# Performance work log

Hardware: AMD Instinct MI355X
Metric: run time of the kernel (lower is better)

Reference implementation:

```python
import jax, jax.numpy as jnp
import numpy as np

H = 512
W = 512
N_STROKES = 5000
S = 10          # samples_per_curve
K = 20          # strokes_per_pixel
CANVAS_COLOR = 0.5  # 'gray'
COARSE = 5      # coarse grid downsample factor (H//5, W//5)


def setup_inputs() -> dict:
    key = jax.random.key(0)
    ks = jax.random.split(key, 6)
    # stroke centers spread over the canvas
    location = jax.random.uniform(ks[0], (N_STROKES, 2), jnp.float32) * jnp.array([H, W], jnp.float32)
    # bezier control-point offsets relative to the stroke center
    curve_s = jax.random.normal(ks[1], (N_STROKES, 2), jnp.float32) * 8.0
    curve_e = jax.random.normal(ks[2], (N_STROKES, 2), jnp.float32) * 8.0
    curve_c = jax.random.normal(ks[3], (N_STROKES, 2), jnp.float32) * 8.0
    color = jax.random.uniform(ks[4], (N_STROKES, 3), jnp.float32)
    width = jax.random.uniform(ks[5], (N_STROKES, 1), jnp.float32) * 4.0 + 1.0
    return {"curve_s": curve_s, "curve_e": curve_e, "curve_c": curve_c,
            "color": color, "location": location, "width": width}


def _bezier_points(s, c, e, num_points):
    # s, c, e: [N, 2] -> [N, num_points, 2]
    t = jnp.linspace(0.0, 1.0, num_points).astype(jnp.float32)  # [S]
    omt2 = (1.0 - t) ** 2  # [S]
    t2 = t ** 2
    # x/y computed identically: c + (1-t)^2 (s - c) + t^2 (e - c)
    pts = c[:, None, :] + omt2[None, :, None] * (s - c)[:, None, :] \
          + t2[None, :, None] * (e - c)[:, None, :]
    return pts  # [N, S, 2]


def _nearest_upsample_idx(out_size, in_size):
    # torch F.interpolate mode='nearest': src = floor(dst * in/out)
    idx = jnp.floor(jnp.arange(out_size) * (in_size / out_size)).astype(jnp.int32)
    return jnp.clip(idx, 0, in_size - 1)


def reference(curve_s, curve_e, curve_c, color, location, width):
    # sample bezier curve points (absolute coords)
    pts = _bezier_points(curve_s + location, curve_c + location,
                         curve_e + location, S)  # [N, S, 2]

    # ---- coarse-grid KNN over stroke centers ----
    Hc, Wc = H // COARSE, W // COARSE
    tH = jnp.linspace(0.0, float(H), Hc).astype(jnp.float32)
    tW = jnp.linspace(0.0, float(W), Wc).astype(jnp.float32)
    Px, Py = jnp.meshgrid(tH, tW, indexing='ij')
    P = jnp.stack([Px, Py], axis=-1)  # [Hc, Wc, 2]
    D_centers = jnp.sum(jnp.square(P[:, :, None, :] - location), axis=-1)  # [Hc, Wc, N]
    _, idcs = jax.lax.top_k(-D_centers, K)  # [Hc, Wc, K]

    near_pts = pts[idcs]      # [Hc, Wc, K, S, 2]
    near_col = color[idcs]    # [Hc, Wc, K, 3]
    near_w = width[idcs]      # [Hc, Wc, K, 1]

    # ---- upsample coarse gathers to full res ----
    ih = _nearest_upsample_idx(H, Hc)
    iw = _nearest_upsample_idx(W, Wc)
    near_pts = near_pts[ih][:, iw]   # [H, W, K, S, 2] (nearest)
    near_col = near_col[ih][:, iw]   # [H, W, K, 3]   (nearest)
    # widths: bilinear (align_corners=False, no antialias) per channel
    near_w = jax.image.resize(near_w[..., 0], (H, W, K), method='linear')[..., None]  # [H, W, K, 1]

    # ---- full-res pixel grid ----
    tHf = jnp.linspace(0.0, float(H), H).astype(jnp.float32)
    tWf = jnp.linspace(0.0, float(W), W).astype(jnp.float32)
    Pxf, Pyf = jnp.meshgrid(tHf, tWf, indexing='ij')
    P_full = jnp.stack([Pxf, Pyf], axis=-1)  # [H, W, 2]

    # ---- per-pixel closest point on each polyline segment ----
    a = near_pts[:, :, :, :S - 1, :]              # [H, W, K, S-1, 2]
    b_a = near_pts[:, :, :, 1:, :] - a            # segment direction
    pa = P_full[:, :, None, None, :] - a          # pixel - segment start
    t = jnp.sum(b_a * pa, axis=-1) / jnp.sum(jnp.square(b_a), axis=-1)
    t = jnp.clip(t, 0.0, 1.0)
    closest = a + t[..., None] * b_a
    dist = jnp.sum(jnp.square(P_full[:, :, None, None, :] - closest), axis=-1)  # [H, W, K, S-1]

    D = jnp.min(dist, axis=(-1, -2))  # [H, W]
    min_per_stroke = jnp.min(dist, axis=-1)  # [H, W, K]
    ranking = jax.nn.softmax(100000.0 * (1.0 / (1e-08 + min_per_stroke)), axis=-1)  # [H, W, K]

    I_colors = jnp.einsum('hwkf,hwk->hwf', near_col, ranking)  # [H, W, 3]
    bs = jnp.einsum('hwkf,hwk->hwf', near_w, ranking)          # [H, W, 1]
    bs_mask = jax.nn.sigmoid(bs - D[..., None])
    canvas = jnp.full_like(I_colors, CANVAS_COLOR)
    I = I_colors * bs_mask + (1.0 - bs_mask) * canvas
    return I
```

## Files before the change

### kernel.cpp

```cpp
#include <hip/hip_runtime.h>
#include <math.h>

#define NS 5000
#define SS 10
#define KK 20
#define HC 102
#define NBIN 32
#define BINW 16.0f
#define CAP 192

#define WAVE_SYNC() __asm__ volatile("s_waitcnt lgkmcnt(0)" ::: "memory")

__global__ void prep_kernel(const float* __restrict__ cs, const float* __restrict__ ce,
                            const float* __restrict__ cc, const float* __restrict__ loc,
                            const float* __restrict__ color, const float* __restrict__ width,
                            float* __restrict__ sdata, float4* __restrict__ ctab,
                            int* __restrict__ binCnt) {
    int i = blockIdx.x * 256 + threadIdx.x;
    if (i >= NS) return;
    float lx = loc[i*2+0], ly = loc[i*2+1];
    float sx = cs[i*2+0] + lx, sy = cs[i*2+1] + ly;
    float ex = ce[i*2+0] + lx, ey = ce[i*2+1] + ly;
    float px = cc[i*2+0] + lx, py = cc[i*2+1] + ly;
    float qx[SS], qy[SS];
    #pragma unroll
    for (int j = 0; j < SS; ++j) {
        float tt = (float)j * (1.0f / 9.0f);
        float omt = 1.0f - tt;
        float omt2 = omt * omt, t2 = tt * tt;
        qx[j] = px + omt2 * (sx - px) + t2 * (ex - px);
        qy[j] = py + omt2 * (sy - py) + t2 * (ey - py);
        sdata[i*32 + 2*j + 0] = qx[j];
        sdata[i*32 + 2*j + 1] = qy[j];
    }
    #pragma unroll
    for (int sg = 0; sg < 9; ++sg) {
        float bx = qx[sg+1] - qx[sg], by = qy[sg+1] - qy[sg];
        sdata[i*32 + 20 + sg] = 1.0f / (bx*bx + by*by);
    }
    sdata[i*32 + 29] = 0.0f; sdata[i*32 + 30] = 0.0f; sdata[i*32 + 31] = 0.0f;
    ctab[i] = make_float4(color[i*3+0], color[i*3+1], color[i*3+2], width[i]);
    int b0 = min(max((int)(lx * (1.0f/BINW)), 0), NBIN-1);
    int b1 = min(max((int)(ly * (1.0f/BINW)), 0), NBIN-1);
    atomicAdd(&binCnt[b0*NBIN + b1], 1);
}

__global__ void binscan_kernel(const int* __restrict__ binCnt, int* __restrict__ binStart) {
    __shared__ int wsum[4];
    int t = threadIdx.x;
    int lane = t & 63, w = t >> 6;
    int4 v = ((const int4*)binCnt)[t];
    int s0 = v.x, s1 = s0 + v.y, s2 = s1 + v.z, s3 = s2 + v.w;
    int x = s3;
    #pragma unroll
    for (int off = 1; off < 64; off <<= 1) {
        int y = __shfl_up(x, off, 64);
        if (lane >= off) x += y;
    }
    if (lane == 63) wsum[w] = x;
    __syncthreads();
    int woff = 0;
    #pragma unroll
    for (int i = 0; i < 4; ++i) woff += (i < w) ? wsum[i] : 0;
    int texcl = woff + x - s3;
    binStart[4*t+1] = texcl + s0;
    binStart[4*t+2] = texcl + s1;
    binStart[4*t+3] = texcl + s2;
    binStart[4*t+4] = texcl + s3;
    if (t == 0) binStart[0] = 0;
}

__global__ void binscatter_kernel(const float* __restrict__ loc, const int* __restrict__ binStart,
                                  int* __restrict__ binFill, float2* __restrict__ sxy,
                                  int* __restrict__ sid) {
    int i = blockIdx.x * 256 + threadIdx.x;
    if (i >= NS) return;
    float l0 = loc[i*2+0], l1 = loc[i*2+1];
    int b0 = min(max((int)(l0 * (1.0f/BINW)), 0), NBIN-1);
    int b1 = min(max((int)(l1 * (1.0f/BINW)), 0), NBIN-1);
    int b = b0*NBIN + b1;
    int pos = binStart[b] + atomicAdd(&binFill[b], 1);
    sxy[pos] = make_float2(l0, l1);
    sid[pos] = i;
}

__global__ void __launch_bounds__(256) topk_kernel(const float* __restrict__ loc,
                                                   const float* __restrict__ width,
                                                   const float2* __restrict__ sxy,
                                                   const int* __restrict__ sid,
                                                   const int* __restrict__ binStart,
                                                   int* __restrict__ idcs,
                                                   float* __restrict__ wk) {
    __shared__ unsigned long long sk[4][CAP];
    int w = threadIdx.x >> 6, lane = threadIdx.x & 63;
    int cell = blockIdx.x * 4 + w;
    int ci = cell / HC, cj = cell - ci * HC;
    const float dc = 512.0f / 101.0f;
    float c0 = (float)ci * dc;
    float c1 = (float)cj * dc;
    unsigned long long below = (1ull << lane) - 1ull;

    float R = 30.0f;
    int cnt = 0;
    for (int attempt = 0; attempt < 5; ++attempt) {
        float R2 = R * R;
        int base = 0;
        int by0 = max((int)((c0 - R) * (1.0f/BINW)), 0);
        int by1 = min((int)((c0 + R) * (1.0f/BINW)), NBIN-1);
        int bx0 = max((int)((c1 - R) * (1.0f/BINW)), 0);
        int bx1 = min((int)((c1 + R) * (1.0f/BINW)), NBIN-1);
        for (int by = by0; by <= by1; ++by) {
            int s = binStart[by*NBIN + bx0];
            int e = binStart[by*NBIN + bx1 + 1];
            for (int t0 = s; t0 < e; t0 += 64) {
                int t = t0 + lane;
                int tc = min(t, e - 1);
                float2 p = sxy[tc];
                float dx = c0 - p.x, dy = c1 - p.y;
                float d = dx*dx + dy*dy;
                bool pred = (t < e) && (d < R2);
                unsigned long long mask = __ballot(pred);
                int pos = base + __popcll(mask & below);
                if (pred && pos < CAP)
                    sk[w][pos] = ((unsigned long long)__float_as_uint(d) << 32)
                               | (unsigned int)sid[tc];
                base += __popcll(mask);
            }
        }
        cnt = base;
        if (cnt >= KK) break;
        R *= 1.6f;
    }
    WAVE_SYNC();

    if (cnt >= KK && cnt <= CAP) {
        if (cnt <= 64) {
            unsigned long long k0 = (lane < cnt) ? sk[w][lane] : ~0ull;
            int r0 = 0;
            int j = 0;
            #pragma unroll 1
            for (; j + 4 <= cnt; j += 4) {
                unsigned long long a = sk[w][j],   b = sk[w][j+1];
                unsigned long long c = sk[w][j+2], d = sk[w][j+3];
                r0 += (int)(a < k0) + (int)(b < k0) + (int)(c < k0) + (int)(d < k0);
            }
            for (; j < cnt; ++j) r0 += (int)(sk[w][j] < k0);
            if (r0 < KK && lane < cnt) {
                int idx = (int)(unsigned int)(k0 & 0xffffffffull);
                idcs[cell*KK + r0] = idx;
                wk[cell*KK + r0]   = width[idx];
            }
        } else {
            unsigned long long k0 = (lane       < cnt) ? sk[w][lane]       : ~0ull;
            unsigned long long k1 = (lane + 64  < cnt) ? sk[w][lane + 64]  : ~0ull;
            unsigned long long k2 = (lane + 128 < cnt) ? sk[w][lane + 128] : ~0ull;
            int r0 = 0, r1 = 0, r2 = 0;
            #pragma unroll 1
            for (int j = 0; j < cnt; ++j) {
                unsigned long long a = sk[w][j];
                r0 += (int)(a < k0); r1 += (int)(a < k1); r2 += (int)(a < k2);
            }
            if (r0 < KK && lane < cnt) {
                int idx = (int)(unsigned int)(k0 & 0xffffffffull);
                idcs[cell*KK + r0] = idx;  wk[cell*KK + r0] = width[idx];
            }
            if (r1 < KK && lane + 64 < cnt) {
                int idx = (int)(unsigned int)(k1 & 0xffffffffull);
                idcs[cell*KK + r1] = idx;  wk[cell*KK + r1] = width[idx];
            }
            if (r2 < KK && lane + 128 < cnt) {
                int idx = (int)(unsigned int)(k2 & 0xffffffffull);
                idcs[cell*KK + r2] = idx;  wk[cell*KK + r2] = width[idx];
            }
        }
    } else {
        if (lane == 0) {
            float bd[KK]; int bi[KK];
            for (int k = 0; k < KK; ++k) { bd[k] = 3.4e38f; bi[k] = 0; }
            for (int n = 0; n < NS; ++n) {
                float dx = c0 - loc[n*2+0];
                float dy = c1 - loc[n*2+1];
                float d = dx*dx + dy*dy;
                if (d < bd[KK-1]) {
                    int p = KK - 1;
                    while (p > 0 && bd[p-1] > d) { bd[p] = bd[p-1]; bi[p] = bi[p-1]; --p; }
                    bd[p] = d; bi[p] = n;
                }
            }
            for (int k = 0; k < KK; ++k) {
                idcs[cell*KK + k] = bi[k];
                wk[cell*KK + k]   = width[bi[k]];
            }
        }
    }
}

__global__ void __launch_bounds__(256, 4) render_kernel(const float* __restrict__ sdata,
                                                        const float4* __restrict__ ctab,
                                                        const int* __restrict__ idcs,
                                                        const float* __restrict__ wk,
                                                        float* __restrict__ out) {
    int tt0 = threadIdx.x, lane = tt0 & 63, wq = tt0 >> 6;
    int x = blockIdx.x * 16 + ((wq & 1) << 3) + (lane & 7);
    int y = blockIdx.y * 16 + ((wq >> 1) << 3) + (lane >> 3);
    const float df = 512.0f / 511.0f;
    float p0 = (float)y * df;
    float p1 = (float)x * df;
    int cy = (y * 51) >> 8;
    int cx = (x * 51) >> 8;

    const int4* mip = (const int4*)(idcs + (cy * HC + cx) * KK);
    int4 m0 = mip[0], m1 = mip[1], m2 = mip[2], m3 = mip[3], m4 = mip[4];
    int idxs[KK] = {m0.x,m0.y,m0.z,m0.w, m1.x,m1.y,m1.z,m1.w, m2.x,m2.y,m2.z,m2.w,
                    m3.x,m3.y,m3.z,m3.w, m4.x,m4.y,m4.z,m4.w};

    const float sc = 102.0f / 512.0f;
    float iny = ((float)y + 0.5f) * sc - 0.5f;
    float inx = ((float)x + 0.5f) * sc - 0.5f;
    float y0f = floorf(iny), x0f = floorf(inx);
    float fy = iny - y0f, fx = inx - x0f;
    int y0 = min(max((int)y0f, 0), HC - 1);
    int y1 = min(max((int)y0f + 1, 0), HC - 1);
    int x0 = min(max((int)x0f, 0), HC - 1);
    int x1 = min(max((int)x0f + 1, 0), HC - 1);
    const float* w00 = wk + (y0 * HC + x0) * KK;
    const float* w01 = wk + (y0 * HC + x1) * KK;
    const float* w10 = wk + (y1 * HC + x0) * KK;
    const float* w11 = wk + (y1 * HC + x1) * KK;

    float m = -INFINITY, s = 0.0f;
    float a0 = 0.0f, a1 = 0.0f, a2 = 0.0f, wa = 0.0f;
    float D = INFINITY;

    #pragma unroll 4
    for (int k = 0; k < KK; ++k) {
        const float4* sp = (const float4*)(sdata + idxs[k] * 32);
        float4 f0 = sp[0], f1 = sp[1], f2 = sp[2], f3 = sp[3], f4 = sp[4];
        float4 i0 = sp[5], i1 = sp[6], i2 = sp[7];
        float4 cw = ctab[idxs[k]];
        float qx[10] = {f0.x, f0.z, f1.x, f1.z, f2.x, f2.z, f3.x, f3.z, f4.x, f4.z};
        float qy[10] = {f0.y, f0.w, f1.y, f1.w, f2.y, f2.w, f3.y, f3.w, f4.y, f4.w};
        float iv[9]  = {i0.x, i0.y, i0.z, i0.w, i1.x, i1.y, i1.z, i1.w, i2.x};
        float mink = INFINITY;
        #pragma unroll
        for (int sg = 0; sg < 9; ++sg) {
            float ax = qx[sg], ay = qy[sg];
            float bx = qx[sg+1] - ax, by = qy[sg+1] - ay;
            float pax = p0 - ax, pay = p1 - ay;
            float dot = bx * pax + by * pay;
            float tt = dot * iv[sg];
            tt = fminf(fmaxf(tt, 0.0f), 1.0f);
            float ccx = ax + tt * bx, ccy = ay + tt * by;
            float ddx = p0 - ccx, ddy = p1 - ccy;
            float d = ddx * ddx + ddy * ddy;
            mink = fminf(mink, d);
        }
        D = fminf(D, mink);
        float z = 100000.0f / (1e-8f + mink);
        float wkv = (1.0f - fy) * ((1.0f - fx) * w00[k] + fx * w01[k])
                  +          fy * ((1.0f - fx) * w10[k] + fx * w11[k]);
        float nm  = fmaxf(m, z);
        float scl = __expf(m - nm);
        float e   = __expf(z - nm);
        s  = s  * scl + e;
        a0 = a0 * scl + cw.x * e;
        a1 = a1 * scl + cw.y * e;
        a2 = a2 * scl + cw.z * e;
        wa = wa * scl + wkv  * e;
        m = nm;
    }
    float inv = 1.0f / s;
    float bs = wa * inv;
    float msk = 1.0f / (1.0f + __expf(-(bs - D)));
    float o0 = a0 * inv * msk + (1.0f - msk) * 0.5f;
    float o1 = a1 * inv * msk + (1.0f - msk) * 0.5f;
    float o2 = a2 * inv * msk + (1.0f - msk) * 0.5f;
    int base = (y * 512 + x) * 3;
    out[base+0] = o0;
    out[base+1] = o1;
    out[base+2] = o2;
}

extern "C" void kernel_launch(void* const* d_in, const int* in_sizes, int n_in,
                              void* d_out, int out_size, void* d_ws, size_t ws_size,
                              hipStream_t stream) {
    const float* cs    = (const float*)d_in[0];
    const float* ce    = (const float*)d_in[1];
    const float* cc    = (const float*)d_in[2];
    const float* color = (const float*)d_in[3];
    const float* loc   = (const float*)d_in[4];
    const float* width = (const float*)d_in[5];
    float* out = (float*)d_out;

    char* p = (char*)d_ws;
    float*  sdata    = (float*)p;                 p += NS * 32 * sizeof(float);
    float4* ctab     = (float4*)p;                p += NS * sizeof(float4);
    int*    idcs     = (int*)p;                   p += (size_t)HC*HC*KK*sizeof(int);
    float*  wk       = (float*)p;                 p += (size_t)HC*HC*KK*sizeof(float);
    int*    binCnt   = (int*)p;                   p += NBIN*NBIN*sizeof(int);
    int*    binFill  = (int*)p;                   p += NBIN*NBIN*sizeof(int);
    int*    binStart = (int*)p;                   p += 4112;
    float2* sxy      = (float2*)p;                p += NS * sizeof(float2);
    int*    sid      = (int*)p;

    hipMemsetAsync(binCnt, 0, 2 * NBIN * NBIN * sizeof(int), stream);

    prep_kernel      <<<(NS + 255) / 256, 256, 0, stream>>>(cs, ce, cc, loc, color, width,
                                                            sdata, ctab, binCnt);
    binscan_kernel   <<<1, 256, 0, stream>>>(binCnt, binStart);
    binscatter_kernel<<<(NS + 255) / 256, 256, 0, stream>>>(loc, binStart, binFill, sxy, sid);
    topk_kernel      <<<(HC*HC)/4, 256, 0, stream>>>(loc, width, sxy, sid, binStart, idcs, wk);
    render_kernel    <<<dim3(32, 32), 256, 0, stream>>>(sdata, ctab, idcs, wk, out);
}
```

Measured before the change: 134.1 us.

## Replace global-atomic binning with per-block histograms and fused scan-scatter

The prep kernel now builds a per-block bin histogram in shared memory and writes it to a per-block slot, which removes the memset of the global counters. The separate scan and scatter kernels are merged: each scatter block sums all per-block histograms, scans them, and computes its own fill offsets in shared memory before placing its strokes. This drops one memset and one kernel launch from the pipeline, at the cost of every scatter block redoing the reduction and scan. Strokes within a bin are now ordered by block, which changes the within-bin order relative to the old global atomics.

```diff
diff --git a/kernel.cpp b/kernel.cpp
--- a/kernel.cpp
+++ b/kernel.cpp
@@ -7,50 +7,68 @@
 #define HC 102
 #define NBIN 32
 #define BINW 16.0f
+#define NPB 20
 #define CAP 192
 
 #define WAVE_SYNC() __asm__ volatile("s_waitcnt lgkmcnt(0)" ::: "memory")
 
-__global__ void prep_kernel(const float* __restrict__ cs, const float* __restrict__ ce,
-                            const float* __restrict__ cc, const float* __restrict__ loc,
-                            const float* __restrict__ color, const float* __restrict__ width,
-                            float* __restrict__ sdata, float4* __restrict__ ctab,
-                            int* __restrict__ binCnt) {
-    int i = blockIdx.x * 256 + threadIdx.x;
-    if (i >= NS) return;
-    float lx = loc[i*2+0], ly = loc[i*2+1];
-    float sx = cs[i*2+0] + lx, sy = cs[i*2+1] + ly;
-    float ex = ce[i*2+0] + lx, ey = ce[i*2+1] + ly;
-    float px = cc[i*2+0] + lx, py = cc[i*2+1] + ly;
-    float qx[SS], qy[SS];
-    #pragma unroll
-    for (int j = 0; j < SS; ++j) {
-        float tt = (float)j * (1.0f / 9.0f);
-        float omt = 1.0f - tt;
-        float omt2 = omt * omt, t2 = tt * tt;
-        qx[j] = px + omt2 * (sx - px) + t2 * (ex - px);
-        qy[j] = py + omt2 * (sy - py) + t2 * (ey - py);
-        sdata[i*32 + 2*j + 0] = qx[j];
-        sdata[i*32 + 2*j + 1] = qy[j];
-    }
-    #pragma unroll
-    for (int sg = 0; sg < 9; ++sg) {
-        float bx = qx[sg+1] - qx[sg], by = qy[sg+1] - qy[sg];
-        sdata[i*32 + 20 + sg] = 1.0f / (bx*bx + by*by);
-    }
-    sdata[i*32 + 29] = 0.0f; sdata[i*32 + 30] = 0.0f; sdata[i*32 + 31] = 0.0f;
-    ctab[i] = make_float4(color[i*3+0], color[i*3+1], color[i*3+2], width[i]);
-    int b0 = min(max((int)(lx * (1.0f/BINW)), 0), NBIN-1);
-    int b1 = min(max((int)(ly * (1.0f/BINW)), 0), NBIN-1);
-    atomicAdd(&binCnt[b0*NBIN + b1], 1);
-}
-
-__global__ void binscan_kernel(const int* __restrict__ binCnt, int* __restrict__ binStart) {
+__global__ void __launch_bounds__(256) prep_kernel(
+        const float* __restrict__ cs, const float* __restrict__ ce,
+        const float* __restrict__ cc, const float* __restrict__ loc,
+        const float* __restrict__ color, const float* __restrict__ width,
+        float* __restrict__ sdata, float4* __restrict__ ctab,
+        int* __restrict__ binCntP) {
+    __shared__ int4 lcnt4[NBIN*NBIN/4];
+    int* lcnt = (int*)lcnt4;
+    int t = threadIdx.x;
+    lcnt4[t] = make_int4(0, 0, 0, 0);
+    __syncthreads();
+    int i = blockIdx.x * 256 + t;
+    if (i < NS) {
+        float lx = loc[i*2+0], ly = loc[i*2+1];
+        float sx = cs[i*2+0] + lx, sy = cs[i*2+1] + ly;
+        float ex = ce[i*2+0] + lx, ey = ce[i*2+1] + ly;
+        float px = cc[i*2+0] + lx, py = cc[i*2+1] + ly;
+        float qx[SS], qy[SS];
+        #pragma unroll
+        for (int j = 0; j < SS; ++j) {
+            float tt = (float)j * (1.0f / 9.0f);
+            float omt = 1.0f - tt;
+            float omt2 = omt * omt, t2 = tt * tt;
+            qx[j] = px + omt2 * (sx - px) + t2 * (ex - px);
+            qy[j] = py + omt2 * (sy - py) + t2 * (ey - py);
+            sdata[i*32 + 2*j + 0] = qx[j];
+            sdata[i*32 + 2*j + 1] = qy[j];
+        }
+        #pragma unroll
+        for (int sg = 0; sg < 9; ++sg) {
+            float bx = qx[sg+1] - qx[sg], by = qy[sg+1] - qy[sg];
+            sdata[i*32 + 20 + sg] = 1.0f / (bx*bx + by*by);
+        }
+        sdata[i*32 + 29] = 0.0f; sdata[i*32 + 30] = 0.0f; sdata[i*32 + 31] = 0.0f;
+        ctab[i] = make_float4(color[i*3+0], color[i*3+1], color[i*3+2], width[i]);
+        int b0 = min(max((int)(lx * (1.0f/BINW)), 0), NBIN-1);
+        int b1 = min(max((int)(ly * (1.0f/BINW)), 0), NBIN-1);
+        atomicAdd(&lcnt[b0*NBIN + b1], 1);
+    }
+    __syncthreads();
+    ((int4*)binCntP)[blockIdx.x * 256 + t] = lcnt4[t];
+}
+
+__global__ void __launch_bounds__(256) scatter_kernel(
+        const float* __restrict__ loc, const int* __restrict__ binCntP,
+        int* __restrict__ binStart, float2* __restrict__ sxy, int* __restrict__ sid) {
+    __shared__ int fill[NBIN*NBIN];
     __shared__ int wsum[4];
-    int t = threadIdx.x;
-    int lane = t & 63, w = t >> 6;
-    int4 v = ((const int4*)binCnt)[t];
-    int s0 = v.x, s1 = s0 + v.y, s2 = s1 + v.z, s3 = s2 + v.w;
+    int t = threadIdx.x, lane = t & 63, w = t >> 6;
+    int mb = blockIdx.x;
+    int4 tot = make_int4(0,0,0,0), bel = make_int4(0,0,0,0);
+    for (int b = 0; b < NPB; ++b) {
+        int4 v = ((const int4*)binCntP)[b * 256 + t];
+        tot.x += v.x; tot.y += v.y; tot.z += v.z; tot.w += v.w;
+        if (b < mb) { bel.x += v.x; bel.y += v.y; bel.z += v.z; bel.w += v.w; }
+    }
+    int s0 = tot.x, s1 = s0 + tot.y, s2 = s1 + tot.z, s3 = s2 + tot.w;
     int x = s3;
     #pragma unroll
     for (int off = 1; off < 64; off <<= 1) {
@@ -63,25 +81,27 @@
     #pragma unroll
     for (int i = 0; i < 4; ++i) woff += (i < w) ? wsum[i] : 0;
     int texcl = woff + x - s3;
-    binStart[4*t+1] = texcl + s0;
-    binStart[4*t+2] = texcl + s1;
-    binStart[4*t+3] = texcl + s2;
-    binStart[4*t+4] = texcl + s3;
-    if (t == 0) binStart[0] = 0;
-}
-
-__global__ void binscatter_kernel(const float* __restrict__ loc, const int* __restrict__ binStart,
-                                  int* __restrict__ binFill, float2* __restrict__ sxy,
-                                  int* __restrict__ sid) {
-    int i = blockIdx.x * 256 + threadIdx.x;
-    if (i >= NS) return;
-    float l0 = loc[i*2+0], l1 = loc[i*2+1];
-    int b0 = min(max((int)(l0 * (1.0f/BINW)), 0), NBIN-1);
-    int b1 = min(max((int)(l1 * (1.0f/BINW)), 0), NBIN-1);
-    int b = b0*NBIN + b1;
-    int pos = binStart[b] + atomicAdd(&binFill[b], 1);
-    sxy[pos] = make_float2(l0, l1);
-    sid[pos] = i;
+    fill[4*t+0] = texcl      + bel.x;
+    fill[4*t+1] = texcl + s0 + bel.y;
+    fill[4*t+2] = texcl + s1 + bel.z;
+    fill[4*t+3] = texcl + s2 + bel.w;
+    if (mb == 0) {
+        binStart[4*t+1] = texcl + s0;
+        binStart[4*t+2] = texcl + s1;
+        binStart[4*t+3] = texcl + s2;
+        binStart[4*t+4] = texcl + s3;
+        if (t == 0) binStart[0] = 0;
+    }
+    __syncthreads();
+    int i = mb * 256 + t;
+    if (i < NS) {
+        float l0 = loc[i*2+0], l1 = loc[i*2+1];
+        int b0 = min(max((int)(l0 * (1.0f/BINW)), 0), NBIN-1);
+        int b1 = min(max((int)(l1 * (1.0f/BINW)), 0), NBIN-1);
+        int pos = atomicAdd(&fill[b0*NBIN + b1], 1);
+        sxy[pos] = make_float2(l0, l1);
+        sid[pos] = i;
+    }
 }
 
 __global__ void __launch_bounds__(256) topk_kernel(const float* __restrict__ loc,
@@ -297,18 +317,13 @@
     float4* ctab     = (float4*)p;                p += NS * sizeof(float4);
     int*    idcs     = (int*)p;                   p += (size_t)HC*HC*KK*sizeof(int);
     float*  wk       = (float*)p;                 p += (size_t)HC*HC*KK*sizeof(float);
-    int*    binCnt   = (int*)p;                   p += NBIN*NBIN*sizeof(int);
-    int*    binFill  = (int*)p;                   p += NBIN*NBIN*sizeof(int);
+    int*    binCntP  = (int*)p;                   p += NPB * NBIN*NBIN * sizeof(int);
     int*    binStart = (int*)p;                   p += 4112;
     float2* sxy      = (float2*)p;                p += NS * sizeof(float2);
     int*    sid      = (int*)p;
 
-    hipMemsetAsync(binCnt, 0, 2 * NBIN * NBIN * sizeof(int), stream);
-
-    prep_kernel      <<<(NS + 255) / 256, 256, 0, stream>>>(cs, ce, cc, loc, color, width,
-                                                            sdata, ctab, binCnt);
-    binscan_kernel   <<<1, 256, 0, stream>>>(binCnt, binStart);
-    binscatter_kernel<<<(NS + 255) / 256, 256, 0, stream>>>(loc, binStart, binFill, sxy, sid);
-    topk_kernel      <<<(HC*HC)/4, 256, 0, stream>>>(loc, width, sxy, sid, binStart, idcs, wk);
-    render_kernel    <<<dim3(32, 32), 256, 0, stream>>>(sdata, ctab, idcs, wk, out);
-}
+    prep_kernel   <<<NPB, 256, 0, stream>>>(cs, ce, cc, loc, color, width, sdata, ctab, binCntP);
+    scatter_kernel<<<NPB, 256, 0, stream>>>(loc, binCntP, binStart, sxy, sid);
+    topk_kernel   <<<(HC*HC)/4, 256, 0, stream>>>(loc, width, sxy, sid, binStart, idcs, wk);
+    render_kernel <<<dim3(32, 32), 256, 0, stream>>>(sdata, ctab, idcs, wk, out);
+}
```

Result: no change. 131.6 us (-1.9%).
